# Performance work log

Hardware: AMD Instinct MI355X
Metric: run time of the kernel (lower is better)

The kernel has to match this reference:

```python
import jax, jax.numpy as jnp
import numpy as np

B, N, DIN, DM, NH = 8, 2048, 256, 256, 4
DK = DM // NH


def setup_inputs() -> dict:
    key = jax.random.key(0)
    ks = jax.random.split(key, 8)
    x = jax.random.normal(ks[0], (B, N, DIN), dtype=jnp.float32)
    # contiguous valid ranges per sample (padding on both ends), matching
    # the module's assumption that torch.where(mask)[0][0]/[−1] define a span
    starts = jax.random.randint(ks[1], (B,), 0, N // 8)
    lens = jax.random.randint(ks[2], (B,), N // 2, N - N // 8)
    pos = jnp.arange(N)
    attention_mask = ((pos[None, :] >= starts[:, None])
                      & (pos[None, :] < starts[:, None] + lens[:, None])).astype(jnp.int32)
    s = 0.02
    Wq = jax.random.normal(ks[3], (DIN, DM), jnp.float32) * s
    Wk = jax.random.normal(ks[4], (DIN, DM), jnp.float32) * s
    Wv = jax.random.normal(ks[5], (DIN, DM), jnp.float32) * s
    Wo = jax.random.normal(ks[6], (DM, DM), jnp.float32) * s
    bq = jnp.zeros((DM,), jnp.float32)
    bk = jnp.zeros((DM,), jnp.float32)
    bv = jnp.zeros((DM,), jnp.float32)
    bo = jnp.zeros((DM,), jnp.float32)
    return {"x": x, "attention_mask": attention_mask,
            "Wq": Wq, "bq": bq, "Wk": Wk, "bk": bk,
            "Wv": Wv, "bv": bv, "Wo": Wo, "bo": bo}


def reference(x, attention_mask, Wq, bq, Wk, bk, Wv, bv, Wo, bo):
    b, n, _ = x.shape
    nh, dk = NH, DK
    scale = 1.0 / np.sqrt(dk)
    q = (x @ Wq + bq).reshape(b, n, nh, dk).transpose(0, 2, 1, 3)  # [b,h,n,dk]
    k = (x @ Wk + bk).reshape(b, n, nh, dk).transpose(0, 2, 1, 3)
    v = (x @ Wv + bv).reshape(b, n, nh, dk).transpose(0, 2, 1, 3)
    dist = jnp.einsum('bhid,bhjd->bhij', q, k) * scale  # [b,h,n,n]

    # Vectorized equivalent of the per-sample python-loop mask:
    # start = first True index; end = last True index (torch slice start:end
    # is EXCLUSIVE of the last valid position -- preserved faithfully).
    m = attention_mask.astype(bool)
    pos = jnp.arange(n)
    start = jnp.argmax(m, axis=1)                      # [b]
    end = n - 1 - jnp.argmax(m[:, ::-1], axis=1)       # [b] last True index
    valid = (pos[None, :] >= start[:, None]) & (pos[None, :] < end[:, None])  # [b,n]
    bias = jnp.where(valid[:, :, None] & valid[:, None, :], 0.0, -1e10)       # [b,n,n]

    dist = jax.nn.softmax(dist + bias[:, None, :, :], axis=-1)
    att = jnp.einsum('bhij,bhjd->bhid', dist, v)       # [b,h,n,dk]
    att = att.transpose(0, 2, 1, 3).reshape(b, n, nh * dk)
    return att @ Wo + bo
```

## Files before the change

kernel.cpp:

```cpp
#include <hip/hip_runtime.h>
#include <hip/hip_bf16.h>
#include <math.h>

namespace {
constexpr int Bb  = 8;
constexpr int Nn  = 2048;
constexpr int DIN_ = 256;
constexpr int DM_  = 256;
constexpr int NH_  = 4;
constexpr int DK_  = 64;
constexpr int BH_  = Bb * NH_;
constexpr float SCALE = 0.125f;
}

typedef __attribute__((ext_vector_type(8))) _Float16 half8;
typedef __attribute__((ext_vector_type(2))) __fp16 fp16x2;
typedef __attribute__((ext_vector_type(4))) float f32x4;

static __device__ __forceinline__ unsigned pkrtz_u32(float a, float b) {
    union { fp16x2 h; unsigned u; } u;
    u.h = __builtin_amdgcn_cvt_pkrtz(a, b);
    return u.u;
}

static __device__ __forceinline__ half8 h8_from_u32x4(unsigned w0, unsigned w1,
                                                      unsigned w2, unsigned w3) {
    union { unsigned u[4]; half8 h; } u;
    u.u[0] = w0; u.u[1] = w1; u.u[2] = w2; u.u[3] = w3;
    return u.h;
}

__global__ __launch_bounds__(256) void prep_kernel(
    const int* __restrict__ mask, int* __restrict__ bounds,
    const float* __restrict__ W0, const float* __restrict__ W1,
    const float* __restrict__ W2, const float* __restrict__ W3,
    _Float16* __restrict__ T0, _Float16* __restrict__ T1,
    _Float16* __restrict__ T2, _Float16* __restrict__ T3)
{
    const int bid = blockIdx.x;
    const int tid = threadIdx.x;
    if (bid < 8) {
        const int b = bid;
        __shared__ int smin[256], smax[256];
        int lmin = Nn, lmax = -1;
        for (int i = tid; i < Nn; i += 256) {
            if (mask[b * Nn + i]) {
                if (i < lmin) lmin = i;
                if (i > lmax) lmax = i;
            }
        }
        smin[tid] = lmin; smax[tid] = lmax;
        __syncthreads();
        for (int s = 128; s > 0; s >>= 1) {
            if (tid < s) {
                smin[tid] = min(smin[tid], smin[tid + s]);
                smax[tid] = max(smax[tid], smax[tid + s]);
            }
            __syncthreads();
        }
        if (tid == 0) { bounds[b * 2] = smin[0]; bounds[b * 2 + 1] = smax[0]; }
    } else {
        const int lin = bid - 8;
        const int wsel = lin >> 6;
        const float* W; _Float16* T;
        switch (wsel) {
            case 0: W = W0; T = T0; break;
            case 1: W = W1; T = T1; break;
            case 2: W = W2; T = T2; break;
            default: W = W3; T = T3; break;
        }
        const int idx = (lin & 63) * 256 + tid;
        const int n = idx & 255;
        const int k0 = (idx >> 8) << 2;
        _Float16 h4[4];
        #pragma unroll
        for (int j = 0; j < 4; ++j) h4[j] = (_Float16)W[(size_t)(k0 + j) * 256 + n];
        *(uint2*)&T[(size_t)n * 256 + k0] = *(const uint2*)h4;
    }
}

__global__ __launch_bounds__(256) void qkv_mfma(
    const float* __restrict__ x,
    const _Float16* __restrict__ Wtq, const float* __restrict__ bq,
    const _Float16* __restrict__ Wtk, const float* __restrict__ bk,
    const _Float16* __restrict__ Wtv, const float* __restrict__ bv,
    _Float16* __restrict__ Qh, _Float16* __restrict__ Kh, _Float16* __restrict__ Vt)
{
    const int zsel = blockIdx.y >> 2;
    const int n0 = (blockIdx.y & 3) * 64;
    const int m0 = blockIdx.x * 128;
    const _Float16* Wt; const float* bias;
    if (zsel == 0)      { Wt = Wtq; bias = bq; }
    else if (zsel == 1) { Wt = Wtk; bias = bk; }
    else                { Wt = Wtv; bias = bv; }

    const int tid = threadIdx.x;
    const int w = tid >> 6, lane = tid & 63;
    const int a = lane & 15, g = lane >> 4;
    const int b = m0 >> 11;

    __shared__ __align__(16) _Float16 As[128 * 64];
    __shared__ __align__(16) _Float16 Bs[64 * 64];

    f32x4 acc[4][2] = {{{0,0,0,0},{0,0,0,0}},{{0,0,0,0},{0,0,0,0}},
                       {{0,0,0,0},{0,0,0,0}},{{0,0,0,0},{0,0,0,0}}};

    for (int step = 0; step < 4; ++step) {
        const int k0 = step * 64;
        {
            const int rb = tid >> 3, fc = tid & 7;
            #pragma unroll
            for (int p = 0; p < 4; ++p) {
                const int row = p * 32 + rb;
                const float4 v0 = *(const float4*)&x[(size_t)(m0 + row) * 256 + k0 + fc * 8];
                const float4 v1 = *(const float4*)&x[(size_t)(m0 + row) * 256 + k0 + fc * 8 + 4];
                _Float16 h[8];
                h[0]=(_Float16)v0.x; h[1]=(_Float16)v0.y; h[2]=(_Float16)v0.z; h[3]=(_Float16)v0.w;
                h[4]=(_Float16)v1.x; h[5]=(_Float16)v1.y; h[6]=(_Float16)v1.z; h[7]=(_Float16)v1.w;
                const int byo = (fc * 16) ^ ((row & 7) << 4);
                *(uint4*)((char*)As + row * 128 + byo) = *(const uint4*)h;
            }
        }
        #pragma unroll
        for (int i = 0; i < 2; ++i) {
            const int f = 2 * w + i;
            const int rowl = f * 8 + (lane >> 3);
            const int byo = ((lane & 7) * 16) ^ ((rowl & 7) << 4);
            const char* src = (const char*)(Wt + (size_t)(n0 + rowl) * 256 + k0) + byo;
            __builtin_amdgcn_global_load_lds(
                (const __attribute__((address_space(1))) void*)src,
                (__attribute__((address_space(3))) void*)((char*)Bs + f * 1024), 16, 0, 0);
        }
        __syncthreads();

        #pragma unroll
        for (int kc = 0; kc < 2; ++kc) {
            half8 xf[2], wf[4];
            #pragma unroll
            for (int tt = 0; tt < 2; ++tt) {
                const int row = 32 * w + 16 * tt + a;
                const int byo = (kc * 64 + g * 16) ^ ((row & 7) << 4);
                xf[tt] = *(const half8*)((const char*)As + row * 128 + byo);
            }
            #pragma unroll
            for (int nf = 0; nf < 4; ++nf) {
                const int row = 16 * nf + a;
                const int byo = (kc * 64 + g * 16) ^ ((row & 7) << 4);
                wf[nf] = *(const half8*)((const char*)Bs + row * 128 + byo);
            }
            if (zsel < 2) {
                #pragma unroll
                for (int nf = 0; nf < 4; ++nf)
                    #pragma unroll
                    for (int tt = 0; tt < 2; ++tt)
                        acc[nf][tt] = __builtin_amdgcn_mfma_f32_16x16x32_f16(wf[nf], xf[tt], acc[nf][tt], 0,0,0);
            } else {
                #pragma unroll
                for (int nf = 0; nf < 4; ++nf)
                    #pragma unroll
                    for (int tt = 0; tt < 2; ++tt)
                        acc[nf][tt] = __builtin_amdgcn_mfma_f32_16x16x32_f16(xf[tt], wf[nf], acc[nf][tt], 0,0,0);
            }
        }
        __syncthreads();
    }

    if (zsel < 2) {
        _Float16* out = zsel ? Kh : Qh;
        #pragma unroll
        for (int nf = 0; nf < 4; ++nf) {
            const int nb = n0 + 16 * nf + 4 * g;
            const f32x4 bi = *(const f32x4*)&bias[nb];
            const int h = nb >> 6, dkb = nb & 63;
            #pragma unroll
            for (int tt = 0; tt < 2; ++tt) {
                const int tok = (m0 + 32 * w + 16 * tt + a) & 2047;
                const f32x4 d = acc[nf][tt];
                _Float16 q4[4];
                q4[0] = (_Float16)(d[0] + bi[0]);
                q4[1] = (_Float16)(d[1] + bi[1]);
                q4[2] = (_Float16)(d[2] + bi[2]);
                q4[3] = (_Float16)(d[3] + bi[3]);
                *(uint2*)&out[(((size_t)(b * NH_ + h)) * Nn + tok) * DK_ + dkb] = *(const uint2*)q4;
            }
        }
    } else {
        const int h = n0 >> 6;
        #pragma unroll
        for (int nf = 0; nf < 4; ++nf) {
            const int n = n0 + 16 * nf + a;
            const float bs = bias[n];
            const int dk = 16 * nf + a;
            #pragma unroll
            for (int tt = 0; tt < 2; ++tt) {
                const int tokb = (m0 + 32 * w + 16 * tt + 4 * g) & 2047;
                const f32x4 d = acc[nf][tt];
                uint2 pk;
                pk.x = pkrtz_u32(d[0] + bs, d[1] + bs);
                pk.y = pkrtz_u32(d[2] + bs, d[3] + bs);
                *(uint2*)&Vt[(((size_t)(b * NH_ + h)) * DK_ + dk) * Nn + tokb] = pk;
            }
        }
    }
}

__global__ __launch_bounds__(256) void colmean_kernel(const _Float16* __restrict__ Vt,
                                                      float* __restrict__ cm) {
    const int bh = blockIdx.x;
    const int t = threadIdx.x;
    const int d = t >> 2, part = t & 3;
    const _Float16* src = Vt + ((size_t)bh * DK_ + d) * Nn + part * 512;
    float s = 0.f;
    for (int i = 0; i < 512; i += 8) {
        half8 v = *(const half8*)(src + i);
        #pragma unroll
        for (int j = 0; j < 8; ++j) s += (float)v[j];
    }
    __shared__ float red[64][4];
    red[d][part] = s;
    __syncthreads();
    if (part == 0)
        cm[bh * DK_ + d] = (red[d][0] + red[d][1] + red[d][2] + red[d][3]) * (1.0f / 2048.0f);
}

__global__ __launch_bounds__(256) void flash_mfma(
    const _Float16* __restrict__ Q, const _Float16* __restrict__ K,
    const _Float16* __restrict__ Vt, const int* __restrict__ bounds,
    _Float16* __restrict__ Oh, float* __restrict__ lw)
{
    const int bid = blockIdx.x;
    const int xcd = bid & 7;
    const int rest = bid >> 3;
    const int qb  = rest & 31;
    const int j   = (rest >> 5) & 3;
    const int s   = rest >> 7;
    const int bh  = j * 8 + xcd;
    const int b  = bh >> 2, h = bh & 3;
    const int q0 = qb * 64;
    const int tid  = threadIdx.x;
    const int w    = tid >> 6;
    const int lane = tid & 63;
    const int a = lane & 15, g = lane >> 4;
    const int start = bounds[2 * b], endv = bounds[2 * b + 1];

    if (q0 + 63 < start || q0 >= endv) return;

    __shared__ __align__(16) _Float16 kfr[2][8][512];
    __shared__ __align__(16) _Float16 vfr[2][8][512];

    const _Float16* Qb = Q  + (size_t)bh * Nn * DK_;
    const _Float16* Kb = K  + (size_t)bh * Nn * DK_;
    const _Float16* Vb = Vt + (size_t)bh * DK_ * Nn;

    const int qrow = q0 + 16 * w + a;
    const half8 qf0 = *(const half8*)&Qb[(size_t)qrow * DK_ + 8 * g];
    const half8 qf1 = *(const half8*)&Qb[(size_t)qrow * DK_ + 32 + 8 * g];

    float l_i = 0.0f;
    f32x4 o0 = {0.f,0.f,0.f,0.f}, o1 = {0.f,0.f,0.f,0.f};
    f32x4 o2 = {0.f,0.f,0.f,0.f}, o3 = {0.f,0.f,0.f,0.f};

#define STAGE(cbuf, kt_) do {                                                        \
        _Pragma("unroll")                                                            \
        for (int ff = 0; ff < 2; ++ff) {                                             \
            const int f  = 2 * w + ff;                                               \
            const int tt = f >> 1, cc = f & 1;                                       \
            const _Float16* ks = &Kb[(size_t)((kt_) + 16 * tt + a) * DK_ + 32 * cc + 8 * g]; \
            __builtin_amdgcn_global_load_lds(                                        \
                (const __attribute__((address_space(1))) void*)ks,                   \
                (__attribute__((address_space(3))) void*)&kfr[cbuf][f][0], 16, 0, 0);\
            const _Float16* vs = &Vb[(size_t)(16 * tt + a) * Nn + (kt_) + 32 * cc + 8 * g]; \
            __builtin_amdgcn_global_load_lds(                                        \
                (const __attribute__((address_space(1))) void*)vs,                   \
                (__attribute__((address_space(3))) void*)&vfr[cbuf][f][0], 16, 0, 0);\
        }                                                                            \
    } while (0)

    const int t0 = start >> 6, t1 = (endv + 63) >> 6;
    const int nt = t1 - t0;
    const int n0t = (nt + 1) >> 1;
    const int ts = (s == 0) ? t0 : t0 + n0t;
    const int te = (s == 0) ? t0 + n0t : t1;

    if (ts < te) {
        const int lo = ts * 64, hiend = te * 64;
        int c = 0;
        STAGE(0, lo);

        for (int kt = lo; kt < hiend; kt += 64) {
            const int nxt = kt + 64;
            if (nxt < hiend) {
                STAGE(c ^ 1, nxt);
                asm volatile("s_waitcnt vmcnt(4)" ::: "memory");
            } else {
                asm volatile("s_waitcnt vmcnt(0)" ::: "memory");
            }
            __builtin_amdgcn_s_barrier();

            const _Float16* kf = &kfr[c][0][0];
            const _Float16* vf = &vfr[c][0][0];

            f32x4 st0 = {0.f,0.f,0.f,0.f}, st1 = {0.f,0.f,0.f,0.f};
            f32x4 st2 = {0.f,0.f,0.f,0.f}, st3 = {0.f,0.f,0.f,0.f};
            __builtin_amdgcn_s_setprio(1);
            st0 = __builtin_amdgcn_mfma_f32_16x16x32_f16(*(const half8*)&kf[0*512 + lane*8], qf0, st0, 0,0,0);
            st0 = __builtin_amdgcn_mfma_f32_16x16x32_f16(*(const half8*)&kf[1*512 + lane*8], qf1, st0, 0,0,0);
            st1 = __builtin_amdgcn_mfma_f32_16x16x32_f16(*(const half8*)&kf[2*512 + lane*8], qf0, st1, 0,0,0);
            st1 = __builtin_amdgcn_mfma_f32_16x16x32_f16(*(const half8*)&kf[3*512 + lane*8], qf1, st1, 0,0,0);
            st2 = __builtin_amdgcn_mfma_f32_16x16x32_f16(*(const half8*)&kf[4*512 + lane*8], qf0, st2, 0,0,0);
            st2 = __builtin_amdgcn_mfma_f32_16x16x32_f16(*(const half8*)&kf[5*512 + lane*8], qf1, st2, 0,0,0);
            st3 = __builtin_amdgcn_mfma_f32_16x16x32_f16(*(const half8*)&kf[6*512 + lane*8], qf0, st3, 0,0,0);
            st3 = __builtin_amdgcn_mfma_f32_16x16x32_f16(*(const half8*)&kf[7*512 + lane*8], qf1, st3, 0,0,0);
            __builtin_amdgcn_s_setprio(0);

            float pv[4][4];
            float rsum = 0.0f;
            const bool edge = (kt < start) || (kt + 64 > endv);
            if (edge) {
                #pragma unroll
                for (int t = 0; t < 4; ++t) {
                    const f32x4 sv = (t == 0) ? st0 : (t == 1) ? st1 : (t == 2) ? st2 : st3;
                    #pragma unroll
                    for (int r = 0; r < 4; ++r) {
                        const int col = kt + 16 * t + 4 * g + r;
                        const bool ok = (col >= start) && (col < endv);
                        const float e = ok ? __expf(sv[r] * SCALE) : 0.0f;
                        pv[t][r] = e;
                        rsum += e;
                    }
                }
            } else {
                #pragma unroll
                for (int t = 0; t < 4; ++t) {
                    const f32x4 sv = (t == 0) ? st0 : (t == 1) ? st1 : (t == 2) ? st2 : st3;
                    #pragma unroll
                    for (int r = 0; r < 4; ++r) {
                        const float e = __expf(sv[r] * SCALE);
                        pv[t][r] = e;
                        rsum += e;
                    }
                }
            }
            rsum += __shfl_xor(rsum, 16, 64);
            rsum += __shfl_xor(rsum, 32, 64);
            l_i += rsum;

            unsigned pk[4][2];
            #pragma unroll
            for (int t = 0; t < 4; ++t) {
                pk[t][0] = pkrtz_u32(pv[t][0], pv[t][1]);
                pk[t][1] = pkrtz_u32(pv[t][2], pv[t][3]);
            }
            const int gsel = g >> 1;
            unsigned aw[2][4];
            #pragma unroll
            for (int cq = 0; cq < 2; ++cq) {
                #pragma unroll
                for (int wd = 0; wd < 4; ++wd) {
                    const int srcLane = a + 16 * (2 * (g & 1) + (wd >> 1));
                    const int lo2 = __shfl((int)pk[2 * cq    ][wd & 1], srcLane, 64);
                    const int hi2 = __shfl((int)pk[2 * cq + 1][wd & 1], srcLane, 64);
                    aw[cq][wd] = (unsigned)(gsel ? hi2 : lo2);
                }
            }
            const half8 pa0 = h8_from_u32x4(aw[0][0], aw[0][1], aw[0][2], aw[0][3]);
            const half8 pa1 = h8_from_u32x4(aw[1][0], aw[1][1], aw[1][2], aw[1][3]);

            __builtin_amdgcn_s_setprio(1);
            o0 = __builtin_amdgcn_mfma_f32_16x16x32_f16(pa0, *(const half8*)&vf[0*512 + lane*8], o0, 0,0,0);
            o0 = __builtin_amdgcn_mfma_f32_16x16x32_f16(pa1, *(const half8*)&vf[1*512 + lane*8], o0, 0,0,0);
            o1 = __builtin_amdgcn_mfma_f32_16x16x32_f16(pa0, *(const half8*)&vf[2*512 + lane*8], o1, 0,0,0);
            o1 = __builtin_amdgcn_mfma_f32_16x16x32_f16(pa1, *(const half8*)&vf[3*512 + lane*8], o1, 0,0,0);
            o2 = __builtin_amdgcn_mfma_f32_16x16x32_f16(pa0, *(const half8*)&vf[4*512 + lane*8], o2, 0,0,0);
            o2 = __builtin_amdgcn_mfma_f32_16x16x32_f16(pa1, *(const half8*)&vf[5*512 + lane*8], o2, 0,0,0);
            o3 = __builtin_amdgcn_mfma_f32_16x16x32_f16(pa0, *(const half8*)&vf[6*512 + lane*8], o3, 0,0,0);
            o3 = __builtin_amdgcn_mfma_f32_16x16x32_f16(pa1, *(const half8*)&vf[7*512 + lane*8], o3, 0,0,0);
            __builtin_amdgcn_s_setprio(0);

            asm volatile("" ::: "memory");
            __builtin_amdgcn_s_barrier();
            c ^= 1;
        }
    }
#undef STAGE

    const size_t half = (size_t)Bb * Nn * DM_;
    _Float16* ob = Oh + (size_t)s * half + ((size_t)b * Nn) * DM_ + h * DK_;
    #pragma unroll
    for (int td = 0; td < 4; ++td) {
        const f32x4 ov = (td == 0) ? o0 : (td == 1) ? o1 : (td == 2) ? o2 : o3;
        #pragma unroll
        for (int r = 0; r < 4; ++r) {
            const int qr = q0 + 16 * w + 4 * g + r;
            ob[(size_t)qr * DM_ + 16 * td + a] = (_Float16)ov[r];
        }
    }
    if (g == 0) {
        const int tok = q0 + 16 * w + a;
        lw[(size_t)s * BH_ * Nn + (size_t)bh * Nn + tok] = l_i;
    }
}

__global__ __launch_bounds__(256) void combine_kernel(
    const _Float16* __restrict__ Oh, const float* __restrict__ lw,
    const int* __restrict__ bounds, const float* __restrict__ cm,
    _Float16* __restrict__ att)
{
    const int b  = blockIdx.y;
    const int q0 = blockIdx.x * 64;
    const int t  = threadIdx.x;
    const int row = q0 + (t >> 2);
    const int h   = t & 3;
    const int c0  = h * 64;
    const int start = bounds[2 * b], endv = bounds[2 * b + 1];
    const bool valid = (row >= start) && (row < endv);

    const size_t half = (size_t)Bb * Nn * DM_;
    const size_t rowoff = ((size_t)b * Nn + row) * DM_ + c0;

    float inv = 0.0f;
    if (valid) {
        const int bh = b * NH_ + h;
        const float l0 = lw[(size_t)bh * Nn + row];
        const float l1 = lw[(size_t)BH_ * Nn + (size_t)bh * Nn + row];
        inv = 1.0f / (l0 + l1);
    }

    #pragma unroll
    for (int jj = 0; jj < 64; jj += 8) {
        _Float16 o[8];
        if (valid) {
            half8 a0 = *(const half8*)&Oh[rowoff + jj];
            half8 a1 = *(const half8*)&Oh[half + rowoff + jj];
            #pragma unroll
            for (int k = 0; k < 8; ++k)
                o[k] = (_Float16)(((float)a0[k] + (float)a1[k]) * inv);
        } else {
            #pragma unroll
            for (int k = 0; k < 8; ++k)
                o[k] = (_Float16)cm[b * DM_ + c0 + jj + k];
        }
        *(uint4*)&att[rowoff + jj] = *(const uint4*)o;
    }
}

__global__ __launch_bounds__(256) void proj_mfma(
    const _Float16* __restrict__ A, const _Float16* __restrict__ Wt,
    const float* __restrict__ bias, float* __restrict__ out)
{
    const int m0 = blockIdx.x * 128;
    const int n0 = blockIdx.y * 64;
    const int tid = threadIdx.x;
    const int w = tid >> 6, lane = tid & 63;
    const int a = lane & 15, g = lane >> 4;

    __shared__ __align__(16) _Float16 As[128 * 64];
    __shared__ __align__(16) _Float16 Bs[64 * 64];

    f32x4 acc[2][4] = {{{0,0,0,0},{0,0,0,0},{0,0,0,0},{0,0,0,0}},
                       {{0,0,0,0},{0,0,0,0},{0,0,0,0},{0,0,0,0}}};

    for (int step = 0; step < 4; ++step) {
        const int k0 = step * 64;
        #pragma unroll
        for (int i = 0; i < 4; ++i) {
            const int f = 4 * w + i;
            const int rowl = f * 8 + (lane >> 3);
            const int byo = ((lane & 7) * 16) ^ ((rowl & 7) << 4);
            const char* src = (const char*)(A + (size_t)(m0 + rowl) * 256 + k0) + byo;
            __builtin_amdgcn_global_load_lds(
                (const __attribute__((address_space(1))) void*)src,
                (__attribute__((address_space(3))) void*)((char*)As + f * 1024), 16, 0, 0);
        }
        #pragma unroll
        for (int i = 0; i < 2; ++i) {
            const int f = 2 * w + i;
            const int rowl = f * 8 + (lane >> 3);
            const int byo = ((lane & 7) * 16) ^ ((rowl & 7) << 4);
            const char* src = (const char*)(Wt + (size_t)(n0 + rowl) * 256 + k0) + byo;
            __builtin_amdgcn_global_load_lds(
                (const __attribute__((address_space(1))) void*)src,
                (__attribute__((address_space(3))) void*)((char*)Bs + f * 1024), 16, 0, 0);
        }
        __syncthreads();

        #pragma unroll
        for (int kc = 0; kc < 2; ++kc) {
            half8 af[2], wf[4];
            #pragma unroll
            for (int tt = 0; tt < 2; ++tt) {
                const int row = 32 * w + 16 * tt + a;
                const int byo = (kc * 64 + g * 16) ^ ((row & 7) << 4);
                af[tt] = *(const half8*)((const char*)As + row * 128 + byo);
            }
            #pragma unroll
            for (int nf = 0; nf < 4; ++nf) {
                const int row = 16 * nf + a;
                const int byo = (kc * 64 + g * 16) ^ ((row & 7) << 4);
                wf[nf] = *(const half8*)((const char*)Bs + row * 128 + byo);
            }
            #pragma unroll
            for (int tt = 0; tt < 2; ++tt)
                #pragma unroll
                for (int nf = 0; nf < 4; ++nf)
                    acc[tt][nf] = __builtin_amdgcn_mfma_f32_16x16x32_f16(af[tt], wf[nf], acc[tt][nf], 0,0,0);
        }
        __syncthreads();
    }

    #pragma unroll
    for (int tt = 0; tt < 2; ++tt) {
        #pragma unroll
        for (int nf = 0; nf < 4; ++nf) {
            const int n = n0 + 16 * nf + a;
            const float bs = bias[n];
            const f32x4 d = acc[tt][nf];
            const int mrow = m0 + 32 * w + 16 * tt + 4 * g;
            #pragma unroll
            for (int r = 0; r < 4; ++r)
                out[(size_t)(mrow + r) * 256 + n] = d[r] + bs;
        }
    }
}

extern "C" void kernel_launch(void* const* d_in, const int* in_sizes, int n_in,
                              void* d_out, int out_size, void* d_ws, size_t ws_size,
                              hipStream_t stream)
{
    const float* x    = (const float*)d_in[0];
    const int*   mask = (const int*)d_in[1];
    const float* Wq   = (const float*)d_in[2];
    const float* bq   = (const float*)d_in[3];
    const float* Wk   = (const float*)d_in[4];
    const float* bk   = (const float*)d_in[5];
    const float* Wv   = (const float*)d_in[6];
    const float* bv   = (const float*)d_in[7];
    const float* Wo   = (const float*)d_in[8];
    const float* bo   = (const float*)d_in[9];
    float* out = (float*)d_out;

    char* ws = (char*)d_ws;
    size_t off = 0;
    int* bounds = (int*)ws;                 off += 256;
    float* cmv  = (float*)(ws + off);       off += (size_t)BH_ * DK_ * sizeof(float);
    off = (off + 255) & ~(size_t)255;
    float* lw   = (float*)(ws + off);       off += (size_t)2 * BH_ * Nn * sizeof(float);
    const size_t h16_bytes = (size_t)BH_ * Nn * DK_ * sizeof(_Float16);
    _Float16* Qh  = (_Float16*)(ws + off); off += h16_bytes;
    _Float16* Kh  = (_Float16*)(ws + off); off += h16_bytes;
    _Float16* Vt  = (_Float16*)(ws + off); off += h16_bytes;
    _Float16* Oh  = (_Float16*)(ws + off); off += 2 * h16_bytes;
    _Float16* ath = (_Float16*)(ws + off); off += h16_bytes;
    _Float16* Wtq = (_Float16*)(ws + off); off += 256 * 256 * sizeof(_Float16);
    _Float16* Wtk = (_Float16*)(ws + off); off += 256 * 256 * sizeof(_Float16);
    _Float16* Wtv = (_Float16*)(ws + off); off += 256 * 256 * sizeof(_Float16);
    _Float16* Wto = (_Float16*)(ws + off); off += 256 * 256 * sizeof(_Float16);

    prep_kernel<<<264, 256, 0, stream>>>(mask, bounds, Wq, Wk, Wv, Wo,
                                         Wtq, Wtk, Wtv, Wto);

    dim3 g1(128, 12);
    qkv_mfma<<<g1, 256, 0, stream>>>(x, Wtq, bq, Wtk, bk, Wtv, bv, Qh, Kh, Vt);

    colmean_kernel<<<BH_, 256, 0, stream>>>(Vt, cmv);

    flash_mfma<<<2048, 256, 0, stream>>>(Qh, Kh, Vt, bounds, Oh, lw);

    dim3 gc(Nn / 64, Bb);
    combine_kernel<<<gc, 256, 0, stream>>>(Oh, lw, bounds, cmv, ath);

    dim3 g3(128, 4);
    proj_mfma<<<g3, 256, 0, stream>>>(ath, Wto, bo, out);
}
```

Baseline: 183.9 us.

## Fuse V column-mean into QKV epilogue and split-combine into output projection

The V column sums are now accumulated with shuffles and atomics in the QKV GEMM epilogue, which removes the separate colmean kernel that re-read Vt. The combine step, which merges the two flash splits, normalizes by the summed l and fills masked rows with the column mean, now runs inside the projection GEMM's A-tile load. That removes a kernel and the att intermediate round-trip through memory. In exchange, the projection loads A through registers instead of async global-to-LDS copies and reads both Oh halves, and the atomic float sums make the column mean non-deterministic.

Result: faster. 168.7 us (-8.3%).

```diff
diff --git a/kernel.cpp b/kernel.cpp
--- a/kernel.cpp
+++ b/kernel.cpp
@@ -32,6 +32,7 @@
 
 __global__ __launch_bounds__(256) void prep_kernel(
     const int* __restrict__ mask, int* __restrict__ bounds,
+    float* __restrict__ cmsum,
     const float* __restrict__ W0, const float* __restrict__ W1,
     const float* __restrict__ W2, const float* __restrict__ W3,
     _Float16* __restrict__ T0, _Float16* __restrict__ T1,
@@ -40,6 +41,7 @@
     const int bid = blockIdx.x;
     const int tid = threadIdx.x;
     if (bid < 8) {
+        cmsum[bid * 256 + tid] = 0.0f;
         const int b = bid;
         __shared__ int smin[256], smax[256];
         int lmin = Nn, lmax = -1;
@@ -84,7 +86,8 @@
     const _Float16* __restrict__ Wtq, const float* __restrict__ bq,
     const _Float16* __restrict__ Wtk, const float* __restrict__ bk,
     const _Float16* __restrict__ Wtv, const float* __restrict__ bv,
-    _Float16* __restrict__ Qh, _Float16* __restrict__ Kh, _Float16* __restrict__ Vt)
+    _Float16* __restrict__ Qh, _Float16* __restrict__ Kh, _Float16* __restrict__ Vt,
+    float* __restrict__ cmsum)
 {
     const int zsel = blockIdx.y >> 2;
     const int n0 = (blockIdx.y & 3) * 64;
@@ -191,36 +194,23 @@
             const int n = n0 + 16 * nf + a;
             const float bs = bias[n];
             const int dk = 16 * nf + a;
+            float csum = 8.0f * bs;
             #pragma unroll
             for (int tt = 0; tt < 2; ++tt) {
                 const int tokb = (m0 + 32 * w + 16 * tt + 4 * g) & 2047;
                 const f32x4 d = acc[nf][tt];
+                csum += d[0] + d[1] + d[2] + d[3];
                 uint2 pk;
                 pk.x = pkrtz_u32(d[0] + bs, d[1] + bs);
                 pk.y = pkrtz_u32(d[2] + bs, d[3] + bs);
                 *(uint2*)&Vt[(((size_t)(b * NH_ + h)) * DK_ + dk) * Nn + tokb] = pk;
             }
-        }
-    }
-}
-
-__global__ __launch_bounds__(256) void colmean_kernel(const _Float16* __restrict__ Vt,
-                                                      float* __restrict__ cm) {
-    const int bh = blockIdx.x;
-    const int t = threadIdx.x;
-    const int d = t >> 2, part = t & 3;
-    const _Float16* src = Vt + ((size_t)bh * DK_ + d) * Nn + part * 512;
-    float s = 0.f;
-    for (int i = 0; i < 512; i += 8) {
-        half8 v = *(const half8*)(src + i);
-        #pragma unroll
-        for (int j = 0; j < 8; ++j) s += (float)v[j];
-    }
-    __shared__ float red[64][4];
-    red[d][part] = s;
-    __syncthreads();
-    if (part == 0)
-        cm[bh * DK_ + d] = (red[d][0] + red[d][1] + red[d][2] + red[d][3]) * (1.0f / 2048.0f);
+            csum += __shfl_xor(csum, 16, 64);
+            csum += __shfl_xor(csum, 32, 64);
+            if (g == 0)
+                atomicAdd(&cmsum[(b * NH_ + h) * DK_ + dk], csum);
+        }
+    }
 }
 
 __global__ __launch_bounds__(256) void flash_mfma(
@@ -401,76 +391,61 @@
     }
 }
 
-__global__ __launch_bounds__(256) void combine_kernel(
+__global__ __launch_bounds__(256) void proj_mfma(
     const _Float16* __restrict__ Oh, const float* __restrict__ lw,
-    const int* __restrict__ bounds, const float* __restrict__ cm,
-    _Float16* __restrict__ att)
-{
-    const int b  = blockIdx.y;
-    const int q0 = blockIdx.x * 64;
-    const int t  = threadIdx.x;
-    const int row = q0 + (t >> 2);
-    const int h   = t & 3;
-    const int c0  = h * 64;
-    const int start = bounds[2 * b], endv = bounds[2 * b + 1];
-    const bool valid = (row >= start) && (row < endv);
-
-    const size_t half = (size_t)Bb * Nn * DM_;
-    const size_t rowoff = ((size_t)b * Nn + row) * DM_ + c0;
-
-    float inv = 0.0f;
-    if (valid) {
-        const int bh = b * NH_ + h;
-        const float l0 = lw[(size_t)bh * Nn + row];
-        const float l1 = lw[(size_t)BH_ * Nn + (size_t)bh * Nn + row];
-        inv = 1.0f / (l0 + l1);
-    }
-
-    #pragma unroll
-    for (int jj = 0; jj < 64; jj += 8) {
-        _Float16 o[8];
-        if (valid) {
-            half8 a0 = *(const half8*)&Oh[rowoff + jj];
-            half8 a1 = *(const half8*)&Oh[half + rowoff + jj];
-            #pragma unroll
-            for (int k = 0; k < 8; ++k)
-                o[k] = (_Float16)(((float)a0[k] + (float)a1[k]) * inv);
-        } else {
-            #pragma unroll
-            for (int k = 0; k < 8; ++k)
-                o[k] = (_Float16)cm[b * DM_ + c0 + jj + k];
-        }
-        *(uint4*)&att[rowoff + jj] = *(const uint4*)o;
-    }
-}
-
-__global__ __launch_bounds__(256) void proj_mfma(
-    const _Float16* __restrict__ A, const _Float16* __restrict__ Wt,
-    const float* __restrict__ bias, float* __restrict__ out)
+    const int* __restrict__ bounds, const float* __restrict__ cmsum,
+    const _Float16* __restrict__ Wt, const float* __restrict__ bias,
+    float* __restrict__ out)
 {
     const int m0 = blockIdx.x * 128;
     const int n0 = blockIdx.y * 64;
     const int tid = threadIdx.x;
     const int w = tid >> 6, lane = tid & 63;
     const int a = lane & 15, g = lane >> 4;
+    const int b = m0 >> 11;
+    const int start = bounds[2 * b], endv = bounds[2 * b + 1];
 
     __shared__ __align__(16) _Float16 As[128 * 64];
     __shared__ __align__(16) _Float16 Bs[64 * 64];
 
+    const size_t half = (size_t)Bb * Nn * DM_;
+
     f32x4 acc[2][4] = {{{0,0,0,0},{0,0,0,0},{0,0,0,0},{0,0,0,0}},
                        {{0,0,0,0},{0,0,0,0},{0,0,0,0},{0,0,0,0}}};
 
     for (int step = 0; step < 4; ++step) {
         const int k0 = step * 64;
-        #pragma unroll
-        for (int i = 0; i < 4; ++i) {
-            const int f = 4 * w + i;
-            const int rowl = f * 8 + (lane >> 3);
-            const int byo = ((lane & 7) * 16) ^ ((rowl & 7) << 4);
-            const char* src = (const char*)(A + (size_t)(m0 + rowl) * 256 + k0) + byo;
-            __builtin_amdgcn_global_load_lds(
-                (const __attribute__((address_space(1))) void*)src,
-                (__attribute__((address_space(3))) void*)((char*)As + f * 1024), 16, 0, 0);
+        {
+            const int rb = tid >> 3, fc = tid & 7;
+            #pragma unroll
+            for (int p = 0; p < 4; ++p) {
+                const int row = p * 32 + rb;
+                const int tok = (m0 + row) & 2047;
+                const bool valid = (tok >= start) && (tok < endv);
+                const size_t rowoff = ((size_t)b * Nn + tok) * DM_ + k0 + fc * 8;
+                _Float16 h[8];
+                if (valid) {
+                    const int bh = b * NH_ + step;
+                    const float l0 = lw[(size_t)bh * Nn + tok];
+                    const float l1 = lw[(size_t)BH_ * Nn + (size_t)bh * Nn + tok];
+                    const float inv = 1.0f / (l0 + l1);
+                    half8 a0 = *(const half8*)&Oh[rowoff];
+                    half8 a1 = *(const half8*)&Oh[half + rowoff];
+                    #pragma unroll
+                    for (int k = 0; k < 8; ++k)
+                        h[k] = (_Float16)(((float)a0[k] + (float)a1[k]) * inv);
+                } else {
+                    const float* cmp = &cmsum[(b * NH_ + step) * DK_ + fc * 8];
+                    const float4 c0 = *(const float4*)cmp;
+                    const float4 c1 = *(const float4*)(cmp + 4);
+                    h[0]=(_Float16)(c0.x*(1.0f/2048.0f)); h[1]=(_Float16)(c0.y*(1.0f/2048.0f));
+                    h[2]=(_Float16)(c0.z*(1.0f/2048.0f)); h[3]=(_Float16)(c0.w*(1.0f/2048.0f));
+                    h[4]=(_Float16)(c1.x*(1.0f/2048.0f)); h[5]=(_Float16)(c1.y*(1.0f/2048.0f));
+                    h[6]=(_Float16)(c1.z*(1.0f/2048.0f)); h[7]=(_Float16)(c1.w*(1.0f/2048.0f));
+                }
+                const int byo = (fc * 16) ^ ((row & 7) << 4);
+                *(uint4*)((char*)As + row * 128 + byo) = *(const uint4*)h;
+            }
         }
         #pragma unroll
         for (int i = 0; i < 2; ++i) {
@@ -542,7 +517,7 @@
     char* ws = (char*)d_ws;
     size_t off = 0;
     int* bounds = (int*)ws;                 off += 256;
-    float* cmv  = (float*)(ws + off);       off += (size_t)BH_ * DK_ * sizeof(float);
+    float* cmsum = (float*)(ws + off);      off += (size_t)BH_ * DK_ * sizeof(float);
     off = (off + 255) & ~(size_t)255;
     float* lw   = (float*)(ws + off);       off += (size_t)2 * BH_ * Nn * sizeof(float);
     const size_t h16_bytes = (size_t)BH_ * Nn * DK_ * sizeof(_Float16);
@@ -550,25 +525,20 @@
     _Float16* Kh  = (_Float16*)(ws + off); off += h16_bytes;
     _Float16* Vt  = (_Float16*)(ws + off); off += h16_bytes;
     _Float16* Oh  = (_Float16*)(ws + off); off += 2 * h16_bytes;
-    _Float16* ath = (_Float16*)(ws + off); off += h16_bytes;
     _Float16* Wtq = (_Float16*)(ws + off); off += 256 * 256 * sizeof(_Float16);
     _Float16* Wtk = (_Float16*)(ws + off); off += 256 * 256 * sizeof(_Float16);
     _Float16* Wtv = (_Float16*)(ws + off); off += 256 * 256 * sizeof(_Float16);
     _Float16* Wto = (_Float16*)(ws + off); off += 256 * 256 * sizeof(_Float16);
 
-    prep_kernel<<<264, 256, 0, stream>>>(mask, bounds, Wq, Wk, Wv, Wo,
+    prep_kernel<<<264, 256, 0, stream>>>(mask, bounds, cmsum, Wq, Wk, Wv, Wo,
                                          Wtq, Wtk, Wtv, Wto);
 
     dim3 g1(128, 12);
-    qkv_mfma<<<g1, 256, 0, stream>>>(x, Wtq, bq, Wtk, bk, Wtv, bv, Qh, Kh, Vt);
-
-    colmean_kernel<<<BH_, 256, 0, stream>>>(Vt, cmv);
+    qkv_mfma<<<g1, 256, 0, stream>>>(x, Wtq, bq, Wtk, bk, Wtv, bv,
+                                     Qh, Kh, Vt, cmsum);
 
     flash_mfma<<<2048, 256, 0, stream>>>(Qh, Kh, Vt, bounds, Oh, lw);
 
-    dim3 gc(Nn / 64, Bb);
-    combine_kernel<<<gc, 256, 0, stream>>>(Oh, lw, bounds, cmv, ath);
-
     dim3 g3(128, 4);
-    proj_mfma<<<g3, 256, 0, stream>>>(ath, Wto, bo, out);
-}
+    proj_mfma<<<g3, 256, 0, stream>>>(Oh, lw, bounds, cmsum, Wto, bo, out);
+}
```
